# Optimization experiments

Hardware: AMD Instinct MI355X
Metric: run time of the kernel (lower is better)

## Reference

```python
import jax, jax.numpy as jnp
import numpy as np

N = 50000       # nodes
E = 800000      # edges (before self loops)
F_IN = 128      # in_channels
HID = 128       # hidden_channels
HEADS = 4
NEG_SLOPE = 0.2  # PyG GATConv default leaky_relu slope


def gat_conv(x, src, dst, W, a_src, a_dst, b, heads, out_ch, concat):
    """PyG-style GATConv (eval mode, dropout off).
    x: [N,F_in]; src/dst: [E'] edge endpoints (edge j->i means src=j, dst=i);
    W: [F_in, heads*out_ch]; a_src,a_dst: [heads,out_ch]; b: [out dim].
    """
    n = x.shape[0]
    h = (x @ W).reshape(n, heads, out_ch)              # [N,H,C]
    alpha_src = jnp.sum(h * a_src, axis=-1)            # [N,H]
    alpha_dst = jnp.sum(h * a_dst, axis=-1)            # [N,H]
    e = jax.nn.leaky_relu(alpha_src[src] + alpha_dst[dst], NEG_SLOPE)  # [E',H]
    # segment softmax over incoming edges of each destination node
    m = jax.ops.segment_max(e, dst, num_segments=n)    # [N,H]
    ex = jnp.exp(e - m[dst])
    den = jax.ops.segment_sum(ex, dst, num_segments=n)
    alpha = ex / den[dst]                              # [E',H]
    out = jax.ops.segment_sum(h[src] * alpha[:, :, None], dst, num_segments=n)  # [N,H,C]
    out = out.reshape(n, heads * out_ch) if concat else out.mean(axis=1)
    return out + b


def setup_inputs() -> dict:
    key = jax.random.key(0)
    ks = jax.random.split(key, 10)
    s = 0.1
    return {
        "x": jax.random.normal(ks[0], (N, F_IN), jnp.float32),
        "edge_index": jax.random.randint(ks[1], (2, E), 0, N),
        # layer 1: heads=4, out_ch=HID//HEADS=32, concat
        "W1": jax.random.normal(ks[2], (F_IN, HID), jnp.float32) * s,
        "att_src1": jax.random.normal(ks[3], (HEADS, HID // HEADS), jnp.float32) * s,
        "att_dst1": jax.random.normal(ks[4], (HEADS, HID // HEADS), jnp.float32) * s,
        "b1": jnp.zeros((HID,), jnp.float32),
        # layer 2: heads=1, out_ch=HID, mean (concat=False)
        "W2": jax.random.normal(ks[5], (HID, HID), jnp.float32) * s,
        "att_src2": jax.random.normal(ks[6], (1, HID), jnp.float32) * s,
        "att_dst2": jax.random.normal(ks[7], (1, HID), jnp.float32) * s,
        "b2": jnp.zeros((HID,), jnp.float32),
    }


def reference(x, edge_index, W1, att_src1, att_dst1, b1, W2, att_src2, att_dst2, b2):
    n = x.shape[0]
    loops = jnp.arange(n, dtype=edge_index.dtype)      # add_self_loops=True (PyG default)
    src = jnp.concatenate([edge_index[0], loops])
    dst = jnp.concatenate([edge_index[1], loops])
    h = gat_conv(x, src, dst, W1, att_src1, att_dst1, b1, HEADS, HID // HEADS, True)
    h = jax.nn.elu(h)                                  # ELU between layers; dropout is identity in eval
    out = gat_conv(h, src, dst, W2, att_src2, att_dst2, b2, 1, HID, False)
    return out
```

## Files before the change

kernel.cpp:

```cpp
#include <hip/hip_runtime.h>
#include <hip/hip_fp16.h>
#include <math.h>

typedef unsigned short u16;
typedef unsigned int u32;
typedef __attribute__((ext_vector_type(8))) _Float16 half8v;
typedef __attribute__((ext_vector_type(4))) float float4v;

#define BKT_SH 7
#define BKT_CAP 4096
#define BKT_MAX 512
#define TILE 4096

__device__ __forceinline__ u16 f2h(float f) {
    __half h = __float2half(f);
    return __half_as_ushort(h);
}

__global__ void prep_w(const float* __restrict__ W1, const float* __restrict__ W2,
                       u16* __restrict__ WT1, u16* __restrict__ WT2,
                       int* __restrict__ bcnt) {
    int t = blockIdx.x * 256 + threadIdx.x;
    if (t < BKT_MAX * 16) bcnt[t] = 0;
    int which = t >> 14, idx = t & 16383;
    int k = idx >> 7, c = idx & 127;
    const float* W = which ? W2 : W1;
    u16* WT = which ? WT2 : WT1;
    WT[c * 128 + k] = f2h(W[k * 128 + c]);
}

template <int IN16, int H>
__global__ __launch_bounds__(256) void gemm_mfma(const void* __restrict__ Xv,
                                                 const u16* __restrict__ WT,
                                                 const float* __restrict__ a_src,
                                                 const float* __restrict__ a_dst,
                                                 u16* __restrict__ Hb,
                                                 float* __restrict__ AS,
                                                 float* __restrict__ AD, int n) {
    __shared__ __align__(16) u16 xs[128][136];
    __shared__ __align__(16) u16 ws[128][136];
    const int t = threadIdx.x;
    const int n0 = blockIdx.x * 128;

    {
        const uint4* src = (const uint4*)WT;
        #pragma unroll
        for (int i = 0; i < 8; ++i) {
            int idx = t + i * 256;
            int row = idx >> 4, oct = idx & 15;
            uint4 v = src[idx];
            *(uint4*)&ws[row][oct * 8] = v;
        }
    }
    if (IN16) {
        const u16* X = (const u16*)Xv;
        #pragma unroll
        for (int i = 0; i < 8; ++i) {
            int idx = t + i * 256;
            int row = idx >> 4, oct = idx & 15;
            uint4 v = make_uint4(0, 0, 0, 0);
            if (n0 + row < n) v = *(const uint4*)&X[(size_t)(n0 + row) * 128 + oct * 8];
            *(uint4*)&xs[row][oct * 8] = v;
        }
    } else {
        const float* X = (const float*)Xv;
        #pragma unroll
        for (int i = 0; i < 16; ++i) {
            int idx = t + i * 256;
            int row = idx >> 5, quad = idx & 31;
            float4 v = make_float4(0.f, 0.f, 0.f, 0.f);
            if (n0 + row < n) v = *(const float4*)&X[(size_t)(n0 + row) * 128 + quad * 4];
            u32 lo = (u32)f2h(v.x) | ((u32)f2h(v.y) << 16);
            u32 hi = (u32)f2h(v.z) | ((u32)f2h(v.w) << 16);
            *(uint2*)&xs[row][quad * 4] = make_uint2(lo, hi);
        }
    }
    __syncthreads();

    const int wave = t >> 6, lane = t & 63;
    const int kcol = lane & 15;
    const int kb = (lane >> 4) * 8;

    #pragma unroll
    for (int tile = 0; tile < 2; ++tile) {
        const int r0 = tile * 64 + wave * 16;
        const int arow = r0 + kcol;

        float4v acc[8];
        #pragma unroll
        for (int j = 0; j < 8; ++j) acc[j] = (float4v){0.f, 0.f, 0.f, 0.f};

        #pragma unroll
        for (int kk = 0; kk < 4; ++kk) {
            const int k0 = kk * 32 + kb;
            half8v a = *(const half8v*)&xs[arow][k0];
            #pragma unroll
            for (int j = 0; j < 8; ++j) {
                half8v b = *(const half8v*)&ws[j * 16 + kcol][k0];
                acc[j] = __builtin_amdgcn_mfma_f32_16x16x32_f16(a, b, acc[j], 0, 0, 0);
            }
        }

        const int rbase = n0 + r0 + (lane >> 4) * 4;
        #pragma unroll
        for (int j = 0; j < 8; ++j) {
            #pragma unroll
            for (int r = 0; r < 4; ++r) {
                int row = rbase + r;
                if (row < n) Hb[(size_t)row * 128 + j * 16 + kcol] = f2h(acc[j][r]);
            }
        }

        float av[8], bv[8];
        #pragma unroll
        for (int j = 0; j < 8; ++j) {
            av[j] = a_src[j * 16 + kcol];
            bv[j] = a_dst[j * 16 + kcol];
        }

        if (H == 4) {
            float ps[4][4], pd[4][4];
            #pragma unroll
            for (int r = 0; r < 4; ++r)
                #pragma unroll
                for (int h = 0; h < 4; ++h) {
                    ps[r][h] = acc[2*h][r] * av[2*h] + acc[2*h+1][r] * av[2*h+1];
                    pd[r][h] = acc[2*h][r] * bv[2*h] + acc[2*h+1][r] * bv[2*h+1];
                }
            #pragma unroll
            for (int o = 8; o >= 1; o >>= 1)
                #pragma unroll
                for (int r = 0; r < 4; ++r)
                    #pragma unroll
                    for (int h = 0; h < 4; ++h) {
                        ps[r][h] += __shfl_xor(ps[r][h], o);
                        pd[r][h] += __shfl_xor(pd[r][h], o);
                    }
            float wvs = 0.f, wvd = 0.f;
            #pragma unroll
            for (int r = 0; r < 4; ++r)
                #pragma unroll
                for (int h = 0; h < 4; ++h)
                    if (kcol == r * 4 + h) { wvs = ps[r][h]; wvd = pd[r][h]; }
            int node = rbase + (kcol >> 2);
            if (node < n) {
                AS[node * 4 + (kcol & 3)] = wvs;
                AD[node * 4 + (kcol & 3)] = wvd;
            }
        } else {
            float ps[4], pd[4];
            #pragma unroll
            for (int r = 0; r < 4; ++r) {
                float s_ = 0.f, d_ = 0.f;
                #pragma unroll
                for (int j = 0; j < 8; ++j) {
                    s_ += acc[j][r] * av[j];
                    d_ += acc[j][r] * bv[j];
                }
                ps[r] = s_; pd[r] = d_;
            }
            #pragma unroll
            for (int o = 8; o >= 1; o >>= 1)
                #pragma unroll
                for (int r = 0; r < 4; ++r) {
                    ps[r] += __shfl_xor(ps[r], o);
                    pd[r] += __shfl_xor(pd[r], o);
                }
            float val = 0.f;
            #pragma unroll
            for (int r = 0; r < 4; ++r)
                if ((kcol & 3) == r) val = (kcol < 4) ? ps[r] : pd[r];
            int node = rbase + (kcol & 3);
            if (kcol < 8 && node < n) {
                if (kcol < 4) AS[node] = val;
                else          AD[node] = val;
            }
        }
    }
}

__global__ __launch_bounds__(256) void bucket_append(
    const int* __restrict__ ei, int* __restrict__ bcnt,
    u32* __restrict__ bkt, int E, int etot, int nbkt) {
    __shared__ u32 ent[TILE];
    __shared__ u16 darr[TILE];
    __shared__ int hist[BKT_MAX], lstart[BKT_MAX], gbase[BKT_MAX], cur[BKT_MAX];
    __shared__ int sc[BKT_MAX];
    const int t = threadIdx.x;
    const int e0 = blockIdx.x * TILE;
    const int cnt = min(TILE, etot - e0);

    for (int i = t; i < BKT_MAX; i += 256) { hist[i] = 0; }
    __syncthreads();

    for (int i = t; i < cnt; i += 256) {
        int e = e0 + i;
        int d = (e < E) ? ei[E + e] : e - E;
        darr[i] = (u16)d;
        atomicAdd(&hist[d >> BKT_SH], 1);
    }
    __syncthreads();

    sc[t] = hist[t];
    sc[t + 256] = hist[t + 256];
    __syncthreads();
    for (int off = 1; off < BKT_MAX; off <<= 1) {
        int i0 = t, i1 = t + 256;
        int v0 = (i0 >= off) ? sc[i0 - off] : 0;
        int v1 = (i1 >= off) ? sc[i1 - off] : 0;
        __syncthreads();
        sc[i0] += v0;
        sc[i1] += v1;
        __syncthreads();
    }
    for (int i = t; i < BKT_MAX; i += 256) {
        int ls = sc[i] - hist[i];
        lstart[i] = ls;
        cur[i] = ls;
        gbase[i] = (i < nbkt && hist[i] > 0) ? atomicAdd(&bcnt[i * 16], hist[i]) : 0;
    }
    __syncthreads();

    for (int i = t; i < cnt; i += 256) {
        int e = e0 + i;
        int s = (e < E) ? ei[e] : e - E;
        int d = darr[i];
        int p = atomicAdd(&cur[d >> BKT_SH], 1);
        ent[p] = ((u32)d << 16) | (u32)s;
    }
    __syncthreads();

    for (int i = t; i < cnt; i += 256) {
        u32 en = ent[i];
        int b = en >> (16 + BKT_SH);
        int pos = gbase[b] + (i - lstart[b]);
        if (pos < BKT_CAP) bkt[(size_t)b * BKT_CAP + pos] = en;
    }
}

__global__ __launch_bounds__(256) void bucket_csr(
    const u32* __restrict__ bkt, const int* __restrict__ bcnt,
    int* __restrict__ offsets, int* __restrict__ csr_src,
    int n, int nbkt, int etot) {
    __shared__ u32 ent[BKT_CAP];
    __shared__ int hist[128], pr[128], cur[128];
    __shared__ int sc[BKT_MAX];
    const int b = blockIdx.x;
    const int t = threadIdx.x;

    sc[t]       = (t < nbkt)       ? min(bcnt[t * 16], BKT_CAP) : 0;
    sc[t + 256] = (t + 256 < nbkt) ? min(bcnt[(t + 256) * 16], BKT_CAP) : 0;
    __syncthreads();
    for (int off = 1; off < BKT_MAX; off <<= 1) {
        int i0 = t, i1 = t + 256;
        int v0 = (i0 >= off) ? sc[i0 - off] : 0;
        int v1 = (i1 >= off) ? sc[i1 - off] : 0;
        __syncthreads();
        sc[i0] += v0;
        sc[i1] += v1;
        __syncthreads();
    }
    const int cnt = min(bcnt[b * 16], BKT_CAP);
    const int base = sc[b] - cnt;
    if (b == 0 && t == 0) offsets[n] = etot;

    for (int i = t; i < cnt; i += 256) ent[i] = bkt[(size_t)b * BKT_CAP + i];
    if (t < 128) hist[t] = 0;
    __syncthreads();
    for (int i = t; i < cnt; i += 256) atomicAdd(&hist[(ent[i] >> 16) & 127], 1);
    __syncthreads();
    if (t < 128) pr[t] = hist[t];
    __syncthreads();
    #pragma unroll
    for (int off = 1; off < 128; off <<= 1) {
        int u = (t >= off && t < 128) ? pr[t - off] : 0;
        __syncthreads();
        if (t < 128) pr[t] += u;
        __syncthreads();
    }
    if (t < 128) {
        int excl = pr[t] - hist[t];
        int d = b * 128 + t;
        if (d < n) offsets[d] = base + excl;
        cur[t] = excl;
    }
    __syncthreads();
    for (int i = t; i < cnt; i += 256) {
        u32 en = ent[i];
        int dl = (en >> 16) & 127;
        int pos = base + atomicAdd(&cur[dl], 1);
        csr_src[pos] = (int)(en & 0xFFFFu);
    }
}

template <int H, int MODE>
__global__ __launch_bounds__(256) void node_fused(
    const int* __restrict__ offsets, const int* __restrict__ csr_src,
    const float* __restrict__ AS, const float* __restrict__ AD,
    const u16* __restrict__ Hb, const float* __restrict__ bias,
    void* __restrict__ OUT, int n) {
    const int wid = threadIdx.x >> 6, lane = threadIdx.x & 63;
    const int d = blockIdx.x * 4 + wid;
    if (d >= n) return;
    const int off = offsets[d];
    const int deg = offsets[d + 1] - off;

    constexpr int SCH = (H == 4) ? 32 : 64;
    const int slot = (H == 4) ? (lane & 15) : lane;
    const int g    = (H == 4) ? (lane >> 4) : 0;
    const float adv = AD[d * H + g];

    const int q  = lane >> 4;
    const int c8 = lane & 15;
    const int ghead = (H == 4) ? (c8 >> 2) : 0;

    float acc[8];
    #pragma unroll
    for (int j = 0; j < 8; ++j) acc[j] = 0.f;
    float smp = 0.f;

    int sA = 0, sB = 0;
    float xA = 0.f, xB = 0.f, vA = 0.f, vB = 0.f;
    {
        int kA = slot; bool a = kA < deg;
        sA = a ? csr_src[off + kA] : 0;
        xA = a ? AS[sA * H + g] : 0.f;
        vA = a ? 1.f : 0.f;
        if (H == 4) {
            int kB = 16 + slot; bool b_ = kB < deg;
            sB = b_ ? csr_src[off + kB] : 0;
            xB = b_ ? AS[sB * H + g] : 0.f;
            vB = b_ ? 1.f : 0.f;
        }
    }

    for (int k0 = 0; k0 < deg; k0 += SCH) {
        float eA = xA + adv; eA = eA > 0.f ? eA : 0.2f * eA;
        float aA = vA * __expf(eA);
        float aB = 0.f;
        if (H == 4) {
            float eB = xB + adv; eB = eB > 0.f ? eB : 0.2f * eB;
            aB = vB * __expf(eB);
        }
        smp += aA + aB;
        const int scA = sA, scB = sB;

        {
            int kA = k0 + SCH + slot; bool a = kA < deg;
            sA = a ? csr_src[off + kA] : 0;
            xA = a ? AS[sA * H + g] : 0.f;
            vA = a ? 1.f : 0.f;
            if (H == 4) {
                int kB = k0 + SCH + 16 + slot; bool b_ = kB < deg;
                sB = b_ ? csr_src[off + kB] : 0;
                xB = b_ ? AS[sB * H + g] : 0.f;
                vB = b_ ? 1.f : 0.f;
            }
        }

        const int rem = min(SCH, deg - k0);
        const int ngr = (rem + 3) >> 2;
        #pragma unroll
        for (int p = 0; p < SCH / 4; ++p) {
            if (p >= ngr) break;
            const int eslot = p * 4 + q;
            float al; int sj;
            if (H == 4) {
                if (p < 4) {
                    al = __shfl(aA, ghead * 16 + eslot);
                    sj = __shfl(scA, ghead * 16 + eslot);
                } else {
                    al = __shfl(aB, ghead * 16 + eslot - 16);
                    sj = __shfl(scB, ghead * 16 + eslot - 16);
                }
            } else {
                al = __shfl(aA, eslot);
                sj = __shfl(scA, eslot);
            }
            uint4 u = *(const uint4*)&Hb[(size_t)sj * 128 + c8 * 8];
            __half2 p0 = *(__half2*)&u.x;
            __half2 p1 = *(__half2*)&u.y;
            __half2 p2 = *(__half2*)&u.z;
            __half2 p3 = *(__half2*)&u.w;
            acc[0] += __low2float(p0) * al; acc[1] += __high2float(p0) * al;
            acc[2] += __low2float(p1) * al; acc[3] += __high2float(p1) * al;
            acc[4] += __low2float(p2) * al; acc[5] += __high2float(p2) * al;
            acc[6] += __low2float(p3) * al; acc[7] += __high2float(p3) * al;
        }
    }

    #pragma unroll
    for (int o = (H == 4 ? 8 : 32); o >= 1; o >>= 1)
        smp += __shfl_xor(smp, o);
    const float den = (H == 4) ? __shfl(smp, ghead * 16) : smp;
    const float dinv = 1.f / den;

    #pragma unroll
    for (int j = 0; j < 8; ++j) {
        acc[j] += __shfl_xor(acc[j], 16);
        acc[j] += __shfl_xor(acc[j], 32);
    }

    if (lane < 16) {
        const float4 bv0 = *(const float4*)&bias[c8 * 8];
        const float4 bv1 = *(const float4*)&bias[c8 * 8 + 4];
        float o_[8];
        o_[0] = acc[0] * dinv + bv0.x; o_[1] = acc[1] * dinv + bv0.y;
        o_[2] = acc[2] * dinv + bv0.z; o_[3] = acc[3] * dinv + bv0.w;
        o_[4] = acc[4] * dinv + bv1.x; o_[5] = acc[5] * dinv + bv1.y;
        o_[6] = acc[6] * dinv + bv1.z; o_[7] = acc[7] * dinv + bv1.w;
        if (MODE == 0) {
            #pragma unroll
            for (int j = 0; j < 8; ++j) o_[j] = o_[j] > 0.f ? o_[j] : expm1f(o_[j]);
            uint4 pk;
            pk.x = (u32)f2h(o_[0]) | ((u32)f2h(o_[1]) << 16);
            pk.y = (u32)f2h(o_[2]) | ((u32)f2h(o_[3]) << 16);
            pk.z = (u32)f2h(o_[4]) | ((u32)f2h(o_[5]) << 16);
            pk.w = (u32)f2h(o_[6]) | ((u32)f2h(o_[7]) << 16);
            *(uint4*)&((u16*)OUT)[(size_t)d * 128 + c8 * 8] = pk;
        } else {
            float* O = (float*)OUT;
            *(float4*)&O[(size_t)d * 128 + c8 * 8]     = make_float4(o_[0], o_[1], o_[2], o_[3]);
            *(float4*)&O[(size_t)d * 128 + c8 * 8 + 4] = make_float4(o_[4], o_[5], o_[6], o_[7]);
        }
    }
}

extern "C" void kernel_launch(void* const* d_in, const int* in_sizes, int n_in,
                              void* d_out, int out_size, void* d_ws, size_t ws_size,
                              hipStream_t stream) {
    const float* x   = (const float*)d_in[0];
    const int*   ei  = (const int*)d_in[1];
    const float* W1  = (const float*)d_in[2];
    const float* as1 = (const float*)d_in[3];
    const float* ad1 = (const float*)d_in[4];
    const float* b1  = (const float*)d_in[5];
    const float* W2  = (const float*)d_in[6];
    const float* as2 = (const float*)d_in[7];
    const float* ad2 = (const float*)d_in[8];
    const float* b2  = (const float*)d_in[9];
    float* out = (float*)d_out;

    const int n = in_sizes[0] / 128;
    const int E = in_sizes[1] / 2;
    const int etot = E + n;
    const int nbkt = (n + 127) >> BKT_SH;

    char* p = (char*)d_ws;
    u16* Hb1 = (u16*)p; p += (size_t)n * 128 * 2;
    u16* Xb2 = (u16*)p; p += (size_t)n * 128 * 2;
    u16* Hb2 = (u16*)p; p += (size_t)n * 128 * 2;
    float* AS = (float*)p; p += (size_t)n * 4 * 4;
    float* AD = (float*)p; p += (size_t)n * 4 * 4;
    u16* WT1 = (u16*)p; p += 32768;
    u16* WT2 = (u16*)p; p += 32768;
    u32* bkt     = (u32*)p; p += (size_t)BKT_MAX * BKT_CAP * 4;
    int* bcnt    = (int*)p; p += (size_t)BKT_MAX * 16 * 4;
    int* csr_src = (int*)p; p += (size_t)etot * 4;
    int* offsets = (int*)p; p += (size_t)(n + 1) * 4;

    const int ggrid = (n + 127) / 128;
    const int ngrid = (n + 3) / 4;
    const int agrid = (etot + TILE - 1) / TILE;

    prep_w<<<128, 256, 0, stream>>>(W1, W2, WT1, WT2, bcnt);
    bucket_append<<<agrid, 256, 0, stream>>>(ei, bcnt, bkt, E, etot, nbkt);
    bucket_csr<<<nbkt, 256, 0, stream>>>(bkt, bcnt, offsets, csr_src, n, nbkt, etot);

    gemm_mfma<0, 4><<<ggrid, 256, 0, stream>>>(x, WT1, as1, ad1, Hb1, AS, AD, n);
    node_fused<4, 0><<<ngrid, 256, 0, stream>>>(offsets, csr_src, AS, AD, Hb1, b1, Xb2, n);

    gemm_mfma<1, 1><<<ggrid, 256, 0, stream>>>(Xb2, WT2, as2, ad2, Hb2, AS, AD, n);
    node_fused<1, 1><<<ngrid, 256, 0, stream>>>(offsets, csr_src, AS, AD, Hb2, b2, out, n);
}
```

Measured before the change: 145.1 us.

## Fuse layer-1 GEMM with edge bucketing and convert weights inside GEMM

Removes the prep_w kernel. Each GEMM block now reads fp32 W and transposes and converts it to fp16 straight into shared memory. The bucket counters are zeroed with hipMemsetAsync, and the layer-1 GEMM and bucket_append run as one launch that splits its blocks between the two roles, so the independent work overlaps and fewer launches are needed. In exchange, every GEMM block repeats the weight conversion with scalar, strided LDS stores. The fused kernel also uses the larger shared-memory footprint for all blocks, which may reduce occupancy for the append blocks.

```diff
diff --git a/kernel.cpp b/kernel.cpp
--- a/kernel.cpp
+++ b/kernel.cpp
@@ -11,46 +11,36 @@
 #define BKT_CAP 4096
 #define BKT_MAX 512
 #define TILE 4096
+#define SMEM_BYTES 69632
 
 __device__ __forceinline__ u16 f2h(float f) {
     __half h = __float2half(f);
     return __half_as_ushort(h);
 }
 
-__global__ void prep_w(const float* __restrict__ W1, const float* __restrict__ W2,
-                       u16* __restrict__ WT1, u16* __restrict__ WT2,
-                       int* __restrict__ bcnt) {
-    int t = blockIdx.x * 256 + threadIdx.x;
-    if (t < BKT_MAX * 16) bcnt[t] = 0;
-    int which = t >> 14, idx = t & 16383;
-    int k = idx >> 7, c = idx & 127;
-    const float* W = which ? W2 : W1;
-    u16* WT = which ? WT2 : WT1;
-    WT[c * 128 + k] = f2h(W[k * 128 + c]);
-}
-
 template <int IN16, int H>
-__global__ __launch_bounds__(256) void gemm_mfma(const void* __restrict__ Xv,
-                                                 const u16* __restrict__ WT,
-                                                 const float* __restrict__ a_src,
-                                                 const float* __restrict__ a_dst,
-                                                 u16* __restrict__ Hb,
-                                                 float* __restrict__ AS,
-                                                 float* __restrict__ AD, int n) {
-    __shared__ __align__(16) u16 xs[128][136];
-    __shared__ __align__(16) u16 ws[128][136];
+__device__ __forceinline__ void do_gemm(char* smem, int bid,
+                                        const void* __restrict__ Xv,
+                                        const float* __restrict__ W,
+                                        const float* __restrict__ a_src,
+                                        const float* __restrict__ a_dst,
+                                        u16* __restrict__ Hb,
+                                        float* __restrict__ AS,
+                                        float* __restrict__ AD, int n) {
+    u16 (*xs)[136] = (u16(*)[136])smem;
+    u16 (*ws)[136] = (u16(*)[136])(smem + 34816);
     const int t = threadIdx.x;
-    const int n0 = blockIdx.x * 128;
-
-    {
-        const uint4* src = (const uint4*)WT;
-        #pragma unroll
-        for (int i = 0; i < 8; ++i) {
-            int idx = t + i * 256;
-            int row = idx >> 4, oct = idx & 15;
-            uint4 v = src[idx];
-            *(uint4*)&ws[row][oct * 8] = v;
-        }
+    const int n0 = bid * 128;
+
+    #pragma unroll
+    for (int i = 0; i < 16; ++i) {
+        int idx = t + i * 256;
+        int k = idx >> 5, c4 = (idx & 31) * 4;
+        float4 v = *(const float4*)&W[k * 128 + c4];
+        ws[c4 + 0][k] = f2h(v.x);
+        ws[c4 + 1][k] = f2h(v.y);
+        ws[c4 + 2][k] = f2h(v.z);
+        ws[c4 + 3][k] = f2h(v.w);
     }
     if (IN16) {
         const u16* X = (const u16*)Xv;
@@ -179,18 +169,23 @@
     }
 }
 
-__global__ __launch_bounds__(256) void bucket_append(
-    const int* __restrict__ ei, int* __restrict__ bcnt,
-    u32* __restrict__ bkt, int E, int etot, int nbkt) {
-    __shared__ u32 ent[TILE];
-    __shared__ u16 darr[TILE];
-    __shared__ int hist[BKT_MAX], lstart[BKT_MAX], gbase[BKT_MAX], cur[BKT_MAX];
-    __shared__ int sc[BKT_MAX];
+__device__ __forceinline__ void do_append(char* smem, int bid,
+                                          const int* __restrict__ ei,
+                                          int* __restrict__ bcnt,
+                                          u32* __restrict__ bkt,
+                                          int E, int etot, int nbkt) {
+    u32* ent   = (u32*)smem;
+    u16* darr  = (u16*)(smem + 16384);
+    int* hist  = (int*)(smem + 24576);
+    int* lstart = hist + BKT_MAX;
+    int* gbase  = lstart + BKT_MAX;
+    int* cur    = gbase + BKT_MAX;
+    int* sc     = cur + BKT_MAX;
     const int t = threadIdx.x;
-    const int e0 = blockIdx.x * TILE;
+    const int e0 = bid * TILE;
     const int cnt = min(TILE, etot - e0);
 
-    for (int i = t; i < BKT_MAX; i += 256) { hist[i] = 0; }
+    for (int i = t; i < BKT_MAX; i += 256) hist[i] = 0;
     __syncthreads();
 
     for (int i = t; i < cnt; i += 256) {
@@ -236,6 +231,28 @@
         int pos = gbase[b] + (i - lstart[b]);
         if (pos < BKT_CAP) bkt[(size_t)b * BKT_CAP + pos] = en;
     }
+}
+
+__global__ __launch_bounds__(256) void k1_fused(
+    const float* __restrict__ x, const float* __restrict__ W1,
+    const float* __restrict__ as1, const float* __restrict__ ad1,
+    u16* __restrict__ Hb1, float* __restrict__ AS, float* __restrict__ AD,
+    const int* __restrict__ ei, int* __restrict__ bcnt, u32* __restrict__ bkt,
+    int E, int etot, int nbkt, int n, int ggrid) {
+    __shared__ __align__(16) char smem[SMEM_BYTES];
+    if ((int)blockIdx.x < ggrid)
+        do_gemm<0, 4>(smem, blockIdx.x, x, W1, as1, ad1, Hb1, AS, AD, n);
+    else
+        do_append(smem, blockIdx.x - ggrid, ei, bcnt, bkt, E, etot, nbkt);
+}
+
+template <int IN16, int H>
+__global__ __launch_bounds__(256) void gemm_only(
+    const void* __restrict__ Xv, const float* __restrict__ W,
+    const float* __restrict__ a_src, const float* __restrict__ a_dst,
+    u16* __restrict__ Hb, float* __restrict__ AS, float* __restrict__ AD, int n) {
+    __shared__ __align__(16) char smem[SMEM_BYTES];
+    do_gemm<IN16, H>(smem, blockIdx.x, Xv, W, a_src, a_dst, Hb, AS, AD, n);
 }
 
 __global__ __launch_bounds__(256) void bucket_csr(
@@ -452,8 +469,6 @@
     u16* Hb2 = (u16*)p; p += (size_t)n * 128 * 2;
     float* AS = (float*)p; p += (size_t)n * 4 * 4;
     float* AD = (float*)p; p += (size_t)n * 4 * 4;
-    u16* WT1 = (u16*)p; p += 32768;
-    u16* WT2 = (u16*)p; p += 32768;
     u32* bkt     = (u32*)p; p += (size_t)BKT_MAX * BKT_CAP * 4;
     int* bcnt    = (int*)p; p += (size_t)BKT_MAX * 16 * 4;
     int* csr_src = (int*)p; p += (size_t)etot * 4;
@@ -463,13 +478,14 @@
     const int ngrid = (n + 3) / 4;
     const int agrid = (etot + TILE - 1) / TILE;
 
-    prep_w<<<128, 256, 0, stream>>>(W1, W2, WT1, WT2, bcnt);
-    bucket_append<<<agrid, 256, 0, stream>>>(ei, bcnt, bkt, E, etot, nbkt);
+    (void)hipMemsetAsync(bcnt, 0, (size_t)BKT_MAX * 16 * 4, stream);
+
+    k1_fused<<<ggrid + agrid, 256, 0, stream>>>(x, W1, as1, ad1, Hb1, AS, AD,
+                                                ei, bcnt, bkt, E, etot, nbkt, n, ggrid);
     bucket_csr<<<nbkt, 256, 0, stream>>>(bkt, bcnt, offsets, csr_src, n, nbkt, etot);
 
-    gemm_mfma<0, 4><<<ggrid, 256, 0, stream>>>(x, WT1, as1, ad1, Hb1, AS, AD, n);
     node_fused<4, 0><<<ngrid, 256, 0, stream>>>(offsets, csr_src, AS, AD, Hb1, b1, Xb2, n);
 
-    gemm_mfma<1, 1><<<ggrid, 256, 0, stream>>>(Xb2, WT2, as2, ad2, Hb2, AS, AD, n);
+    gemm_only<1, 1><<<ggrid, 256, 0, stream>>>(Xb2, W2, as2, ad2, Hb2, AS, AD, n);
     node_fused<1, 1><<<ngrid, 256, 0, stream>>>(offsets, csr_src, AS, AD, Hb2, b2, out, n);
 }
```

New measurement: 157.9 us. +8.9%, slower.
